# Performance work log

Measured on AMD Instinct MI355X. Metric: run time of the kernel, lower is better.

## Reference

```python
import jax, jax.numpy as jnp
import numpy as np

N_NODES = 100000
N_EDGES = 20000
N_PAIRS = 640000
IN_CH = 128
HEADS = 4
OUT_CH = 32


def setup_inputs() -> dict:
    key = jax.random.key(0)
    k1, k2, k3, k4, k5 = jax.random.split(key, 5)
    X = jax.random.normal(k1, (N_NODES, IN_CH), dtype=jnp.float32)
    # nn.Linear(in, H*C, bias=False); stored as [in, H*C] so X0 = X @ W
    W = jax.random.normal(k2, (IN_CH, HEADS * OUT_CH), dtype=jnp.float32) * (1.0 / np.sqrt(IN_CH))
    stdv = (6.0 / (HEADS + OUT_CH)) ** 0.5
    att_e = jax.random.uniform(k3, (1, HEADS, OUT_CH), dtype=jnp.float32, minval=-stdv, maxval=stdv)
    vertex = jax.random.randint(k4, (N_PAIRS,), 0, N_NODES, dtype=jnp.int64)
    edges = jax.random.randint(k5, (N_PAIRS,), 0, N_EDGES, dtype=jnp.int64)
    return {"X": X, "W": W, "att_e": att_e, "vertex": vertex, "edges": edges}


def reference(X, W, att_e, vertex, edges):
    N = X.shape[0]
    H, C = HEADS, OUT_CH
    X0 = X @ W                                  # [N, H*C]
    Xv_hc = X0.reshape(N, H, C)
    Xve = Xv_hc[vertex]                          # [M, H, C] gather
    # scatter-mean over hyperedges
    esum = jax.ops.segment_sum(Xve, edges, num_segments=N_EDGES)
    ecnt = jax.ops.segment_sum(jnp.ones((Xve.shape[0],), X.dtype), edges, num_segments=N_EDGES)
    Xe = esum / jnp.maximum(ecnt, 1.0)[:, None, None]   # [E, H, C]
    alpha_e = (Xe * att_e).sum(-1)               # [E, H]
    a_ev = alpha_e[edges]                        # [M, H]
    alpha = jax.nn.leaky_relu(a_ev, 0.01)
    # per-vertex softmax over incident hyperedges
    amax = jax.ops.segment_max(alpha, vertex, num_segments=N)
    alpha = jnp.exp(alpha - amax[vertex])
    asum = jax.ops.segment_sum(alpha, vertex, num_segments=N)
    alpha = alpha / (asum[vertex] + 1e-8)
    Xev = Xe[edges] * alpha[:, :, None]          # [M, H, C]
    Xv = jax.ops.segment_sum(Xev, vertex, num_segments=N)
    return Xv.reshape(N, H * C) + X0
```

## Files before the change

kernel.cpp:

```cpp
#include <hip/hip_runtime.h>
#include <hip/hip_bf16.h>

#define N_NODES 100000
#define N_EDGES 20000
#define N_PAIRS 640000
#define CH 128
#define HEADS 4
#define MAXDV 32

#define NG_GEMM 1563
#define NCHUNK 125
#define ECHUNK 5120
#define EW 5120
#define VWR 6250
#define NRANGE 4
#define VBIN_R 25000

#define OFF_X0H   0UL
#define OFF_XEH   25600000UL
#define OFF_LRE   30720000UL
#define OFF_LRV   31360000UL
#define OFF_BLKE  32000000UL
#define OFF_BLKV  34560000UL
#define OFF_GSE   47060000UL
#define OFF_GSV   47162400UL
#define OFF_WT    47662400UL
#define OFF_ALPHA 47695168UL
#define OFF_OFFE  48015168UL
#define OFF_ENDE  48097088UL
#define OFF_OFFV  48179008UL
#define OFF_ENDV  48579008UL
#define OFF_PIDXE 48979008UL
#define OFF_PIDXV 51539008UL
#define OFF_CNTE  54099008UL
#define OFF_CNTV  54180928UL
#define OFF_TOT   54580928UL
#define ZERO_BYTES 8UL

typedef __attribute__((ext_vector_type(8))) short bf16x8;
typedef __attribute__((ext_vector_type(4))) float f32x4;

__device__ inline short f2bf(float f) {
    __hip_bfloat16 h = __float2bfloat16(f);
    return reinterpret_cast<short&>(h);
}
__device__ inline float bf2f(short s) {
    unsigned int u = ((unsigned int)(unsigned short)s) << 16;
    union { unsigned int u; float f; } c; c.u = u;
    return c.f;
}

__global__ __launch_bounds__(256) void k_wprep(const float* __restrict__ W,
                                               short* __restrict__ Wt) {
    const int idx = blockIdx.x * 256 + threadIdx.x;
    const int n = idx >> 7, k = idx & 127;
    Wt[n * CH + k] = f2bf(W[k * CH + n]);
}

__device__ inline void gemm_body(int gb, const float* __restrict__ X,
                                 const short* __restrict__ Wt,
                                 short* __restrict__ X0h) {
    const int t = threadIdx.x;
    const int wave = t >> 6, lane = t & 63;
    const int r0 = gb * 64 + (wave >> 1) * 32;
    const int c0 = (wave & 1) * 64;
    const int lrow = lane & 15, lk8 = (lane >> 4) * 8;
    const int row0 = min(r0 + lrow, N_NODES - 1);
    const int row1 = min(r0 + 16 + lrow, N_NODES - 1);
    const float* px0 = &X[(size_t)row0 * CH + lk8];
    const float* px1 = &X[(size_t)row1 * CH + lk8];
    const short* pw0 = &Wt[(size_t)(c0 + lrow) * CH + lk8];

    f32x4 acc[2][4] = {};

    float4 xa[2][2]; bf16x8 bb[4];
    xa[0][0] = *(const float4*)(px0); xa[0][1] = *(const float4*)(px0 + 4);
    xa[1][0] = *(const float4*)(px1); xa[1][1] = *(const float4*)(px1 + 4);
#pragma unroll
    for (int n = 0; n < 4; ++n) bb[n] = *(const bf16x8*)(pw0 + n * 16 * CH);

#pragma unroll
    for (int kk = 0; kk < 4; ++kk) {
        float4 xn[2][2]; bf16x8 bn[4];
        if (kk < 3) {
            const int ks = (kk + 1) * 32;
            xn[0][0] = *(const float4*)(px0 + ks); xn[0][1] = *(const float4*)(px0 + ks + 4);
            xn[1][0] = *(const float4*)(px1 + ks); xn[1][1] = *(const float4*)(px1 + ks + 4);
#pragma unroll
            for (int n = 0; n < 4; ++n) bn[n] = *(const bf16x8*)(pw0 + n * 16 * CH + ks);
        }
        bf16x8 a[2];
#pragma unroll
        for (int m = 0; m < 2; ++m) {
            a[m][0] = f2bf(xa[m][0].x); a[m][1] = f2bf(xa[m][0].y);
            a[m][2] = f2bf(xa[m][0].z); a[m][3] = f2bf(xa[m][0].w);
            a[m][4] = f2bf(xa[m][1].x); a[m][5] = f2bf(xa[m][1].y);
            a[m][6] = f2bf(xa[m][1].z); a[m][7] = f2bf(xa[m][1].w);
        }
#pragma unroll
        for (int m = 0; m < 2; ++m)
#pragma unroll
            for (int n = 0; n < 4; ++n)
                acc[m][n] = __builtin_amdgcn_mfma_f32_16x16x32_bf16(a[m], bb[n], acc[m][n], 0, 0, 0);
        if (kk < 3) {
#pragma unroll
            for (int m = 0; m < 2; ++m) { xa[m][0] = xn[m][0]; xa[m][1] = xn[m][1]; }
#pragma unroll
            for (int n = 0; n < 4; ++n) bb[n] = bn[n];
        }
    }

#pragma unroll
    for (int m = 0; m < 2; ++m) {
#pragma unroll
        for (int reg = 0; reg < 4; ++reg) {
            const int row = r0 + m * 16 + (lane >> 4) * 4 + reg;
            if (row < N_NODES) {
#pragma unroll
                for (int n = 0; n < 4; ++n)
                    X0h[(size_t)row * CH + c0 + n * 16 + (lane & 15)] = f2bf(acc[m][n][reg]);
            }
        }
    }
}

__global__ __launch_bounds__(256) void k_phase1(const float* __restrict__ X,
                                                const short* __restrict__ Wt,
                                                short* __restrict__ X0h,
                                                const int* __restrict__ vertex,
                                                const int* __restrict__ edges,
                                                unsigned char* __restrict__ lrank_e,
                                                unsigned char* __restrict__ lrank_v,
                                                unsigned int* __restrict__ blkcnt_e,
                                                unsigned int* __restrict__ blkcnt_v) {
    __shared__ unsigned int hist[VWR];
    const int bid = blockIdx.x;
    const int t = threadIdx.x;

    if (bid < NRANGE * NCHUNK) {
        const int r = bid & 3, c = bid >> 2;
        for (int i = t; i < VWR; i += 256) hist[i] = 0;
        __syncthreads();
        const int base = c * ECHUNK;
        const int vmin = r * VBIN_R;
#pragma unroll
        for (int it = 0; it < 20; ++it) {
            const int m = base + it * 256 + t;
            const int loc = vertex[m] - vmin;
            if ((unsigned)loc < (unsigned)VBIN_R) {
                const unsigned sh = (unsigned)(loc & 3) * 8u;
                unsigned old = atomicAdd(&hist[loc >> 2], 1u << sh);
                lrank_v[m] = (unsigned char)((old >> sh) & 0xffu);
            }
        }
        __syncthreads();
        unsigned int* dst = &blkcnt_v[(size_t)(r * NCHUNK + c) * VWR];
        for (int w = t; w < VWR; w += 256) dst[w] = hist[w];
        return;
    }
    if (bid < NRANGE * NCHUNK + NCHUNK) {
        const int c = bid - NRANGE * NCHUNK;
        for (int i = t; i < EW; i += 256) hist[i] = 0;
        __syncthreads();
        const int base = c * ECHUNK;
#pragma unroll
        for (int it = 0; it < 20; ++it) {
            const int m = base + it * 256 + t;
            const int e = edges[m];
            const unsigned sh = (unsigned)(e & 3) * 8u;
            unsigned old = atomicAdd(&hist[e >> 2], 1u << sh);
            lrank_e[m] = (unsigned char)((old >> sh) & 0xffu);
        }
        __syncthreads();
        unsigned int* dst = &blkcnt_e[(size_t)c * EW];
        for (int w = t; w < EW; w += 256) dst[w] = hist[w];
        return;
    }
    gemm_body(bid - (NRANGE * NCHUNK + NCHUNK), X, Wt, X0h);
}

__global__ __launch_bounds__(256) void k_scan_p1(const unsigned int* __restrict__ blkcnt_e,
                                                 const unsigned int* __restrict__ blkcnt_v,
                                                 unsigned int* __restrict__ gse,
                                                 unsigned int* __restrict__ gsv) {
    const int bid = blockIdx.x;
    if (bid < 100) {
        const int gid = bid * 256 + threadIdx.x;
        const int g = gid / EW, w = gid % EW;
        unsigned s = 0;
#pragma unroll 5
        for (int i = 0; i < 25; ++i) s += blkcnt_e[(size_t)(g * 25 + i) * EW + w];
        gse[g * EW + w] = s;
        return;
    }
    const int vid = (bid - 100) * 256 + threadIdx.x;
    if (vid >= 20 * VWR) return;
    const int g = vid / VWR, w = vid % VWR;
    const int r = g / 5, cg = g % 5;
    unsigned s = 0;
#pragma unroll 5
    for (int i = 0; i < 25; ++i)
        s += blkcnt_v[(size_t)(r * NCHUNK + cg * 25 + i) * VWR + w];
    gsv[g * VWR + w] = s;
}

__global__ __launch_bounds__(256) void k_scan_p2(unsigned int* __restrict__ gse,
                                                 unsigned int* __restrict__ gsv,
                                                 int* __restrict__ cnt_e,
                                                 int* __restrict__ cnt_v) {
    const int bid = blockIdx.x;
    if (bid < 20) {
        const int w = bid * 256 + threadIdx.x;
        unsigned run = 0;
#pragma unroll
        for (int g = 0; g < 5; ++g) {
            unsigned c = gse[g * EW + w];
            gse[g * EW + w] = run;
            run += c;
        }
        int4 o = { (int)(run & 0xffu), (int)((run >> 8) & 0xffu),
                   (int)((run >> 16) & 0xffu), (int)(run >> 24) };
        *(int4*)&cnt_e[4 * w] = o;
        return;
    }
    const int id = (bid - 20) * 256 + threadIdx.x;
    if (id >= NRANGE * VWR) return;
    const int r = id / VWR, w = id % VWR;
    unsigned run = 0;
#pragma unroll
    for (int g = r * 5; g < r * 5 + 5; ++g) {
        unsigned c = gsv[g * VWR + w];
        gsv[g * VWR + w] = run;
        run += c;
    }
    int4 o = { (int)(run & 0xffu), (int)((run >> 8) & 0xffu),
               (int)((run >> 16) & 0xffu), (int)(run >> 24) };
    *(int4*)&cnt_v[r * VBIN_R + 4 * w] = o;
}

__global__ __launch_bounds__(256) void k_scan_p3(unsigned int* __restrict__ blkcnt_e,
                                                 unsigned int* __restrict__ blkcnt_v,
                                                 const unsigned int* __restrict__ gse,
                                                 const unsigned int* __restrict__ gsv) {
    const int bid = blockIdx.x;
    if (bid < 100) {
        const int gid = bid * 256 + threadIdx.x;
        const int g = gid / EW, w = gid % EW;
        unsigned run = gse[g * EW + w];
#pragma unroll 5
        for (int i = 0; i < 25; ++i) {
            const size_t idx = (size_t)(g * 25 + i) * EW + w;
            unsigned c = blkcnt_e[idx];
            blkcnt_e[idx] = run;
            run += c;
        }
        return;
    }
    const int vid = (bid - 100) * 256 + threadIdx.x;
    if (vid >= 20 * VWR) return;
    const int g = vid / VWR, w = vid % VWR;
    const int r = g / 5, cg = g % 5;
    unsigned run = gsv[g * VWR + w];
#pragma unroll 5
    for (int i = 0; i < 25; ++i) {
        const size_t idx = (size_t)(r * NCHUNK + cg * 25 + i) * VWR + w;
        unsigned c = blkcnt_v[idx];
        blkcnt_v[idx] = run;
        run += c;
    }
}

__global__ __launch_bounds__(256) void k_offsets2(const int* __restrict__ cnt_e,
                                                  int* __restrict__ off_e,
                                                  int* __restrict__ end_e,
                                                  const int* __restrict__ cnt_v,
                                                  int* __restrict__ off_v,
                                                  int* __restrict__ end_v,
                                                  int* __restrict__ totals) {
    __shared__ int s[256];
    __shared__ int base;
    const int bid = blockIdx.x, t = threadIdx.x;
    const int* cnt; int* off; int* end; int* total; int n, i;
    if (bid < 79) { cnt = cnt_e; off = off_e; end = end_e; total = &totals[0]; n = N_EDGES;  i = bid * 256 + t; }
    else          { cnt = cnt_v; off = off_v; end = end_v; total = &totals[1]; n = N_NODES; i = (bid - 79) * 256 + t; }
    const int c = (i < n) ? cnt[i] : 0;
    s[t] = c;
    __syncthreads();
    for (int d = 1; d < 256; d <<= 1) {
        int x = (t >= d) ? s[t - d] : 0;
        __syncthreads();
        s[t] += x;
        __syncthreads();
    }
    if (t == 0) base = atomicAdd(total, s[255]);
    __syncthreads();
    if (i < n) {
        int o = base + s[t] - c;
        off[i] = o;
        end[i] = o + c;
    }
}

__global__ __launch_bounds__(256) void k_scatter(const int* __restrict__ vertex,
                                                 const int* __restrict__ edges,
                                                 const unsigned char* __restrict__ lrank_e,
                                                 const unsigned char* __restrict__ lrank_v,
                                                 const unsigned int* __restrict__ blkcnt_e,
                                                 const unsigned int* __restrict__ blkcnt_v,
                                                 const int* __restrict__ off_e,
                                                 const int* __restrict__ off_v,
                                                 int* __restrict__ vlist_e,
                                                 int* __restrict__ elist_v) {
    const int m = blockIdx.x * 256 + threadIdx.x;
    const int e = edges[m];
    const int v = vertex[m];
    const int c = m / ECHUNK;
    const unsigned pe = blkcnt_e[(size_t)c * EW + (e >> 2)];
    const int er = (int)((pe >> ((unsigned)(e & 3) * 8u)) & 0xffu) + (int)lrank_e[m];
    const int r = v / VBIN_R, loc = v - r * VBIN_R;
    const unsigned pv = blkcnt_v[(size_t)(r * NCHUNK + c) * VWR + (loc >> 2)];
    const int vr = (int)((pv >> ((unsigned)(loc & 3) * 8u)) & 0xffu) + (int)lrank_v[m];
    vlist_e[off_e[e] + er] = v;
    elist_v[off_v[v] + vr] = e;
}

__global__ __launch_bounds__(256) void k_edge(const short* __restrict__ X0h,
                                              const int* __restrict__ off_e,
                                              const int* __restrict__ end_e,
                                              const int* __restrict__ vlist,
                                              const float* __restrict__ att,
                                              short* __restrict__ Xeh,
                                              float* __restrict__ alpha_le) {
    const int t = threadIdx.x;
    const int slot = t >> 5, lane = t & 31;
    const int half = lane >> 4, cl = lane & 15;
    const int e = blockIdx.x * 8 + slot;
    const int s = off_e[e], en = end_e[e];
    const int deg = en - s;

    float va[8] = {0.f, 0.f, 0.f, 0.f, 0.f, 0.f, 0.f, 0.f};
    for (int c0 = 0; c0 < deg; c0 += 32) {
        const int cn = min(32, deg - c0);
        int vl = (lane < cn) ? vlist[s + c0 + lane] : 0;
#pragma unroll 4
        for (int j = 0; j < cn; j += 2) {
            const int jj = j + half;
            const int vj = __shfl(vl, jj, 32);
            if (jj < cn) {
                bf16x8 x = *(const bf16x8*)&X0h[(size_t)vj * CH + cl * 8];
#pragma unroll
                for (int i = 0; i < 8; ++i) va[i] += bf2f(x[i]);
            }
        }
    }
#pragma unroll
    for (int i = 0; i < 8; ++i) va[i] += __shfl_xor(va[i], 16);

    const float invd = 1.0f / fmaxf((float)deg, 1.0f);
    bf16x8 xh;
    float xe[8];
#pragma unroll
    for (int i = 0; i < 8; ++i) { xe[i] = va[i] * invd; xh[i] = f2bf(xe[i]); }
    if (half == 0) *(bf16x8*)&Xeh[(size_t)e * CH + cl * 8] = xh;

    const float4 a0 = *(const float4*)&att[cl * 8];
    const float4 a1 = *(const float4*)&att[cl * 8 + 4];
    float p = xe[0] * a0.x + xe[1] * a0.y + xe[2] * a0.z + xe[3] * a0.w
            + xe[4] * a1.x + xe[5] * a1.y + xe[6] * a1.z + xe[7] * a1.w;
    p += __shfl_xor(p, 1);
    p += __shfl_xor(p, 2);
    if (half == 0 && (cl & 3) == 0) {
        alpha_le[e * HEADS + (cl >> 2)] = (p > 0.f) ? p : 0.01f * p;
    }
}

__global__ __launch_bounds__(256) void k_vertex(const short* __restrict__ X0h,
                                                const short* __restrict__ Xeh,
                                                const float* __restrict__ alpha_le,
                                                const int* __restrict__ off_v,
                                                const int* __restrict__ end_v,
                                                const int* __restrict__ elist,
                                                float* __restrict__ out) {
    const int t = threadIdx.x;
    const int slot = t >> 5, lane = t & 31;
    const int half = lane >> 4, cl = lane & 15, h = cl >> 2;
    const int v = blockIdx.x * 8 + slot;
    const int s = off_v[v], en = end_v[v];
    const int deg = en - s;

    __shared__ int   se[8][MAXDV];
    __shared__ float sa[8][MAXDV * HEADS];

    if (deg <= MAXDV && lane < deg) {
        int e = elist[s + lane];
        se[slot][lane] = e;
        *(float4*)&sa[slot][lane << 2] = *(const float4*)&alpha_le[e * HEADS];
    }
    const bf16x8 resh = *(const bf16x8*)&X0h[(size_t)v * CH + cl * 8];
    __syncthreads();

    float va[8] = {0.f, 0.f, 0.f, 0.f, 0.f, 0.f, 0.f, 0.f};
    if (deg <= MAXDV) {
        float mx = -INFINITY;
        for (int j = 0; j < deg; ++j) mx = fmaxf(mx, sa[slot][(j << 2) + h]);
        float ssum = 0.f;
        for (int j = 0; j < deg; ++j) ssum += __expf(sa[slot][(j << 2) + h] - mx);
        const float inv = 1.0f / (ssum + 1e-8f);
#pragma unroll 2
        for (int j = 0; j < deg; j += 2) {
            const int jj = j + half;
            if (jj < deg) {
                const float w = __expf(sa[slot][(jj << 2) + h] - mx) * inv;
                bf16x8 x = *(const bf16x8*)&Xeh[(size_t)se[slot][jj] * CH + cl * 8];
#pragma unroll
                for (int i = 0; i < 8; ++i) va[i] += w * bf2f(x[i]);
            }
        }
    } else {
        float mx = -INFINITY;
        for (int j = 0; j < deg; ++j) mx = fmaxf(mx, alpha_le[elist[s + j] * HEADS + h]);
        float ssum = 0.f;
        for (int j = 0; j < deg; ++j) ssum += __expf(alpha_le[elist[s + j] * HEADS + h] - mx);
        const float inv = 1.0f / (ssum + 1e-8f);
        for (int j = 0; j < deg; ++j) {
            if (half == 0) {
                const int e = elist[s + j];
                const float w = __expf(alpha_le[e * HEADS + h] - mx) * inv;
                bf16x8 x = *(const bf16x8*)&Xeh[(size_t)e * CH + cl * 8];
#pragma unroll
                for (int i = 0; i < 8; ++i) va[i] += w * bf2f(x[i]);
            }
        }
    }
#pragma unroll
    for (int i = 0; i < 8; ++i) va[i] += __shfl_xor(va[i], 16);

    if (half == 0) {
        float4 o0, o1;
        o0.x = va[0] + bf2f(resh[0]); o0.y = va[1] + bf2f(resh[1]);
        o0.z = va[2] + bf2f(resh[2]); o0.w = va[3] + bf2f(resh[3]);
        o1.x = va[4] + bf2f(resh[4]); o1.y = va[5] + bf2f(resh[5]);
        o1.z = va[6] + bf2f(resh[6]); o1.w = va[7] + bf2f(resh[7]);
        *(float4*)&out[(size_t)v * CH + cl * 8]     = o0;
        *(float4*)&out[(size_t)v * CH + cl * 8 + 4] = o1;
    }
}

extern "C" void kernel_launch(void* const* d_in, const int* in_sizes, int n_in,
                              void* d_out, int out_size, void* d_ws, size_t ws_size,
                              hipStream_t stream) {
    const float* X      = (const float*)d_in[0];
    const float* W      = (const float*)d_in[1];
    const float* att    = (const float*)d_in[2];
    const int*   vertex = (const int*)d_in[3];
    const int*   edges  = (const int*)d_in[4];
    float* out = (float*)d_out;

    char* ws = (char*)d_ws;
    short* X0h      = (short*)(ws + OFF_X0H);
    short* Xeh      = (short*)(ws + OFF_XEH);
    unsigned char* lrank_e = (unsigned char*)(ws + OFF_LRE);
    unsigned char* lrank_v = (unsigned char*)(ws + OFF_LRV);
    unsigned int*  blkcnt_e = (unsigned int*)(ws + OFF_BLKE);
    unsigned int*  blkcnt_v = (unsigned int*)(ws + OFF_BLKV);
    unsigned int*  gse      = (unsigned int*)(ws + OFF_GSE);
    unsigned int*  gsv      = (unsigned int*)(ws + OFF_GSV);
    short* Wt       = (short*)(ws + OFF_WT);
    float* alpha_le = (float*)(ws + OFF_ALPHA);
    int* off_e   = (int*)(ws + OFF_OFFE);
    int* end_e   = (int*)(ws + OFF_ENDE);
    int* off_v   = (int*)(ws + OFF_OFFV);
    int* end_v   = (int*)(ws + OFF_ENDV);
    int* vlist_e = (int*)(ws + OFF_PIDXE);
    int* elist_v = (int*)(ws + OFF_PIDXV);
    int* cnt_e   = (int*)(ws + OFF_CNTE);
    int* cnt_v   = (int*)(ws + OFF_CNTV);
    int* totals  = (int*)(ws + OFF_TOT);

    hipMemsetAsync(ws + OFF_TOT, 0, ZERO_BYTES, stream);

    k_wprep<<<64, 256, 0, stream>>>(W, Wt);
    k_phase1<<<NRANGE * NCHUNK + NCHUNK + NG_GEMM, 256, 0, stream>>>(
        X, Wt, X0h, vertex, edges, lrank_e, lrank_v, blkcnt_e, blkcnt_v);
    k_scan_p1<<<100 + 489, 256, 0, stream>>>(blkcnt_e, blkcnt_v, gse, gsv);
    k_scan_p2<<<20 + 98, 256, 0, stream>>>(gse, gsv, cnt_e, cnt_v);
    k_scan_p3<<<100 + 489, 256, 0, stream>>>(blkcnt_e, blkcnt_v, gse, gsv);
    k_offsets2<<<79 + 391, 256, 0, stream>>>(cnt_e, off_e, end_e, cnt_v, off_v, end_v, totals);
    k_scatter<<<N_PAIRS / 256, 256, 0, stream>>>(vertex, edges, lrank_e, lrank_v,
                                                 blkcnt_e, blkcnt_v, off_e, off_v,
                                                 vlist_e, elist_v);
    k_edge<<<N_EDGES / 8, 256, 0, stream>>>(X0h, off_e, end_e, vlist_e, att, Xeh, alpha_le);
    k_vertex<<<N_NODES / 8, 256, 0, stream>>>(X0h, Xeh, alpha_le, off_v, end_v, elist_v, out);
}
```

Before: 160.6 us.

## Split GEMM from counting kernel and compute vertex softmax with wave shuffles

```diff
diff --git a/kernel.cpp b/kernel.cpp
--- a/kernel.cpp
+++ b/kernel.cpp
@@ -44,10 +44,10 @@
     __hip_bfloat16 h = __float2bfloat16(f);
     return reinterpret_cast<short&>(h);
 }
+__device__ inline float bflo(unsigned w) { return __uint_as_float(w << 16); }
+__device__ inline float bfhi(unsigned w) { return __uint_as_float(w & 0xffff0000u); }
 __device__ inline float bf2f(short s) {
-    unsigned int u = ((unsigned int)(unsigned short)s) << 16;
-    union { unsigned int u; float f; } c; c.u = u;
-    return c.f;
+    return __uint_as_float(((unsigned)(unsigned short)s) << 16);
 }
 
 __global__ __launch_bounds__(256) void k_wprep(const float* __restrict__ W,
@@ -57,12 +57,12 @@
     Wt[n * CH + k] = f2bf(W[k * CH + n]);
 }
 
-__device__ inline void gemm_body(int gb, const float* __restrict__ X,
-                                 const short* __restrict__ Wt,
-                                 short* __restrict__ X0h) {
+__global__ __launch_bounds__(256) void k_gemm(const float* __restrict__ X,
+                                              const short* __restrict__ Wt,
+                                              short* __restrict__ X0h) {
     const int t = threadIdx.x;
     const int wave = t >> 6, lane = t & 63;
-    const int r0 = gb * 64 + (wave >> 1) * 32;
+    const int r0 = blockIdx.x * 64 + (wave >> 1) * 32;
     const int c0 = (wave & 1) * 64;
     const int lrow = lane & 15, lk8 = (lane >> 4) * 8;
     const int row0 = min(r0 + lrow, N_NODES - 1);
@@ -124,15 +124,12 @@
     }
 }
 
-__global__ __launch_bounds__(256) void k_phase1(const float* __restrict__ X,
-                                                const short* __restrict__ Wt,
-                                                short* __restrict__ X0h,
-                                                const int* __restrict__ vertex,
-                                                const int* __restrict__ edges,
-                                                unsigned char* __restrict__ lrank_e,
-                                                unsigned char* __restrict__ lrank_v,
-                                                unsigned int* __restrict__ blkcnt_e,
-                                                unsigned int* __restrict__ blkcnt_v) {
+__global__ __launch_bounds__(256) void k_count(const int* __restrict__ vertex,
+                                               const int* __restrict__ edges,
+                                               unsigned char* __restrict__ lrank_e,
+                                               unsigned char* __restrict__ lrank_v,
+                                               unsigned int* __restrict__ blkcnt_e,
+                                               unsigned int* __restrict__ blkcnt_v) {
     __shared__ unsigned int hist[VWR];
     const int bid = blockIdx.x;
     const int t = threadIdx.x;
@@ -158,25 +155,21 @@
         for (int w = t; w < VWR; w += 256) dst[w] = hist[w];
         return;
     }
-    if (bid < NRANGE * NCHUNK + NCHUNK) {
-        const int c = bid - NRANGE * NCHUNK;
-        for (int i = t; i < EW; i += 256) hist[i] = 0;
-        __syncthreads();
-        const int base = c * ECHUNK;
-#pragma unroll
-        for (int it = 0; it < 20; ++it) {
-            const int m = base + it * 256 + t;
-            const int e = edges[m];
-            const unsigned sh = (unsigned)(e & 3) * 8u;
-            unsigned old = atomicAdd(&hist[e >> 2], 1u << sh);
-            lrank_e[m] = (unsigned char)((old >> sh) & 0xffu);
-        }
-        __syncthreads();
-        unsigned int* dst = &blkcnt_e[(size_t)c * EW];
-        for (int w = t; w < EW; w += 256) dst[w] = hist[w];
-        return;
-    }
-    gemm_body(bid - (NRANGE * NCHUNK + NCHUNK), X, Wt, X0h);
+    const int c = bid - NRANGE * NCHUNK;
+    for (int i = t; i < EW; i += 256) hist[i] = 0;
+    __syncthreads();
+    const int base = c * ECHUNK;
+#pragma unroll
+    for (int it = 0; it < 20; ++it) {
+        const int m = base + it * 256 + t;
+        const int e = edges[m];
+        const unsigned sh = (unsigned)(e & 3) * 8u;
+        unsigned old = atomicAdd(&hist[e >> 2], 1u << sh);
+        lrank_e[m] = (unsigned char)((old >> sh) & 0xffu);
+    }
+    __syncthreads();
+    unsigned int* dst = &blkcnt_e[(size_t)c * EW];
+    for (int w = t; w < EW; w += 256) dst[w] = hist[w];
 }
 
 __global__ __launch_bounds__(256) void k_scan_p1(const unsigned int* __restrict__ blkcnt_e,
@@ -347,9 +340,11 @@
             const int jj = j + half;
             const int vj = __shfl(vl, jj, 32);
             if (jj < cn) {
-                bf16x8 x = *(const bf16x8*)&X0h[(size_t)vj * CH + cl * 8];
-#pragma unroll
-                for (int i = 0; i < 8; ++i) va[i] += bf2f(x[i]);
+                uint4 xq = *(const uint4*)&X0h[(size_t)vj * CH + cl * 8];
+                va[0] += bflo(xq.x); va[1] += bfhi(xq.x);
+                va[2] += bflo(xq.y); va[3] += bfhi(xq.y);
+                va[4] += bflo(xq.z); va[5] += bfhi(xq.z);
+                va[6] += bflo(xq.w); va[7] += bfhi(xq.w);
             }
         }
     }
@@ -391,29 +386,53 @@
     __shared__ int   se[8][MAXDV];
     __shared__ float sa[8][MAXDV * HEADS];
 
-    if (deg <= MAXDV && lane < deg) {
-        int e = elist[s + lane];
-        se[slot][lane] = e;
-        *(float4*)&sa[slot][lane << 2] = *(const float4*)&alpha_le[e * HEADS];
-    }
     const bf16x8 resh = *(const bf16x8*)&X0h[(size_t)v * CH + cl * 8];
-    __syncthreads();
 
     float va[8] = {0.f, 0.f, 0.f, 0.f, 0.f, 0.f, 0.f, 0.f};
     if (deg <= MAXDV) {
-        float mx = -INFINITY;
-        for (int j = 0; j < deg; ++j) mx = fmaxf(mx, sa[slot][(j << 2) + h]);
-        float ssum = 0.f;
-        for (int j = 0; j < deg; ++j) ssum += __expf(sa[slot][(j << 2) + h] - mx);
-        const float inv = 1.0f / (ssum + 1e-8f);
+        float4 al = make_float4(-INFINITY, -INFINITY, -INFINITY, -INFINITY);
+        if (lane < deg) {
+            const int e = elist[s + lane];
+            se[slot][lane] = e;
+            al = *(const float4*)&alpha_le[e * HEADS];
+        }
+        float4 mx = al;
+#pragma unroll
+        for (int msk = 1; msk < 32; msk <<= 1) {
+            mx.x = fmaxf(mx.x, __shfl_xor(mx.x, msk, 32));
+            mx.y = fmaxf(mx.y, __shfl_xor(mx.y, msk, 32));
+            mx.z = fmaxf(mx.z, __shfl_xor(mx.z, msk, 32));
+            mx.w = fmaxf(mx.w, __shfl_xor(mx.w, msk, 32));
+        }
+        float4 p = make_float4(0.f, 0.f, 0.f, 0.f);
+        if (lane < deg) {
+            p.x = __expf(al.x - mx.x); p.y = __expf(al.y - mx.y);
+            p.z = __expf(al.z - mx.z); p.w = __expf(al.w - mx.w);
+        }
+        float4 sm = p;
+#pragma unroll
+        for (int msk = 1; msk < 32; msk <<= 1) {
+            sm.x += __shfl_xor(sm.x, msk, 32);
+            sm.y += __shfl_xor(sm.y, msk, 32);
+            sm.z += __shfl_xor(sm.z, msk, 32);
+            sm.w += __shfl_xor(sm.w, msk, 32);
+        }
+        if (lane < deg) {
+            float4 w4;
+            w4.x = p.x / (sm.x + 1e-8f); w4.y = p.y / (sm.y + 1e-8f);
+            w4.z = p.z / (sm.z + 1e-8f); w4.w = p.w / (sm.w + 1e-8f);
+            *(float4*)&sa[slot][lane << 2] = w4;
+        }
 #pragma unroll 2
         for (int j = 0; j < deg; j += 2) {
             const int jj = j + half;
             if (jj < deg) {
-                const float w = __expf(sa[slot][(jj << 2) + h] - mx) * inv;
-                bf16x8 x = *(const bf16x8*)&Xeh[(size_t)se[slot][jj] * CH + cl * 8];
-#pragma unroll
-                for (int i = 0; i < 8; ++i) va[i] += w * bf2f(x[i]);
+                const float w = sa[slot][(jj << 2) + h];
+                uint4 xq = *(const uint4*)&Xeh[(size_t)se[slot][jj] * CH + cl * 8];
+                va[0] += w * bflo(xq.x); va[1] += w * bfhi(xq.x);
+                va[2] += w * bflo(xq.y); va[3] += w * bfhi(xq.y);
+                va[4] += w * bflo(xq.z); va[5] += w * bfhi(xq.z);
+                va[6] += w * bflo(xq.w); va[7] += w * bfhi(xq.w);
             }
         }
     } else {
@@ -426,9 +445,11 @@
             if (half == 0) {
                 const int e = elist[s + j];
                 const float w = __expf(alpha_le[e * HEADS + h] - mx) * inv;
-                bf16x8 x = *(const bf16x8*)&Xeh[(size_t)e * CH + cl * 8];
-#pragma unroll
-                for (int i = 0; i < 8; ++i) va[i] += w * bf2f(x[i]);
+                uint4 xq = *(const uint4*)&Xeh[(size_t)e * CH + cl * 8];
+                va[0] += w * bflo(xq.x); va[1] += w * bfhi(xq.x);
+                va[2] += w * bflo(xq.y); va[3] += w * bfhi(xq.y);
+                va[4] += w * bflo(xq.z); va[5] += w * bfhi(xq.z);
+                va[6] += w * bflo(xq.w); va[7] += w * bfhi(xq.w);
             }
         }
     }
@@ -480,8 +501,9 @@
     hipMemsetAsync(ws + OFF_TOT, 0, ZERO_BYTES, stream);
 
     k_wprep<<<64, 256, 0, stream>>>(W, Wt);
-    k_phase1<<<NRANGE * NCHUNK + NCHUNK + NG_GEMM, 256, 0, stream>>>(
-        X, Wt, X0h, vertex, edges, lrank_e, lrank_v, blkcnt_e, blkcnt_v);
+    k_count<<<NRANGE * NCHUNK + NCHUNK, 256, 0, stream>>>(
+        vertex, edges, lrank_e, lrank_v, blkcnt_e, blkcnt_v);
+    k_gemm<<<NG_GEMM, 256, 0, stream>>>(X, Wt, X0h);
     k_scan_p1<<<100 + 489, 256, 0, stream>>>(blkcnt_e, blkcnt_v, gse, gsv);
     k_scan_p2<<<20 + 98, 256, 0, stream>>>(gse, gsv, cnt_e, cnt_v);
     k_scan_p3<<<100 + 489, 256, 0, stream>>>(blkcnt_e, blkcnt_v, gse, gsv);
```

New measurement: 168.0 us. +4.7%, slower.

## Fuse offset scan into scan pass 2 and remap vertex kernel to half-warp per vertex

Applied to the files above, without the earlier changes.

```diff
diff --git a/kernel.cpp b/kernel.cpp
--- a/kernel.cpp
+++ b/kernel.cpp
@@ -32,8 +32,6 @@
 #define OFF_ENDV  48579008UL
 #define OFF_PIDXE 48979008UL
 #define OFF_PIDXV 51539008UL
-#define OFF_CNTE  54099008UL
-#define OFF_CNTV  54180928UL
 #define OFF_TOT   54580928UL
 #define ZERO_BYTES 8UL
 
@@ -44,10 +42,10 @@
     __hip_bfloat16 h = __float2bfloat16(f);
     return reinterpret_cast<short&>(h);
 }
+__device__ inline float bflo(unsigned w) { return __uint_as_float(w << 16); }
+__device__ inline float bfhi(unsigned w) { return __uint_as_float(w & 0xffff0000u); }
 __device__ inline float bf2f(short s) {
-    unsigned int u = ((unsigned int)(unsigned short)s) << 16;
-    union { unsigned int u; float f; } c; c.u = u;
-    return c.f;
+    return __uint_as_float(((unsigned)(unsigned short)s) << 16);
 }
 
 __global__ __launch_bounds__(256) void k_wprep(const float* __restrict__ W,
@@ -204,38 +202,67 @@
     gsv[g * VWR + w] = s;
 }
 
-__global__ __launch_bounds__(256) void k_scan_p2(unsigned int* __restrict__ gse,
-                                                 unsigned int* __restrict__ gsv,
-                                                 int* __restrict__ cnt_e,
-                                                 int* __restrict__ cnt_v) {
-    const int bid = blockIdx.x;
+__global__ __launch_bounds__(256) void k_p2o(unsigned int* __restrict__ gse,
+                                             unsigned int* __restrict__ gsv,
+                                             int* __restrict__ off_e,
+                                             int* __restrict__ end_e,
+                                             int* __restrict__ off_v,
+                                             int* __restrict__ end_v,
+                                             int* __restrict__ totals) {
+    __shared__ int s[256];
+    __shared__ int base;
+    const int bid = blockIdx.x, t = threadIdx.x;
+
+    unsigned run = 0;
+    int t0 = 0, t1 = 0, t2 = 0, t3 = 0;
+    int binbase = -1;
+    int* off; int* end; int* total;
+
     if (bid < 20) {
-        const int w = bid * 256 + threadIdx.x;
-        unsigned run = 0;
+        const int w = bid * 256 + t;
 #pragma unroll
         for (int g = 0; g < 5; ++g) {
             unsigned c = gse[g * EW + w];
             gse[g * EW + w] = run;
             run += c;
         }
-        int4 o = { (int)(run & 0xffu), (int)((run >> 8) & 0xffu),
-                   (int)((run >> 16) & 0xffu), (int)(run >> 24) };
-        *(int4*)&cnt_e[4 * w] = o;
-        return;
-    }
-    const int id = (bid - 20) * 256 + threadIdx.x;
-    if (id >= NRANGE * VWR) return;
-    const int r = id / VWR, w = id % VWR;
-    unsigned run = 0;
-#pragma unroll
-    for (int g = r * 5; g < r * 5 + 5; ++g) {
-        unsigned c = gsv[g * VWR + w];
-        gsv[g * VWR + w] = run;
-        run += c;
-    }
-    int4 o = { (int)(run & 0xffu), (int)((run >> 8) & 0xffu),
-               (int)((run >> 16) & 0xffu), (int)(run >> 24) };
-    *(int4*)&cnt_v[r * VBIN_R + 4 * w] = o;
+        t0 = run & 255; t1 = (run >> 8) & 255; t2 = (run >> 16) & 255; t3 = run >> 24;
+        binbase = 4 * w;
+        off = off_e; end = end_e; total = &totals[0];
+    } else {
+        const int id = (bid - 20) * 256 + t;
+        if (id < NRANGE * VWR) {
+            const int r = id / VWR, w = id % VWR;
+#pragma unroll
+            for (int g = r * 5; g < r * 5 + 5; ++g) {
+                unsigned c = gsv[g * VWR + w];
+                gsv[g * VWR + w] = run;
+                run += c;
+            }
+            t0 = run & 255; t1 = (run >> 8) & 255; t2 = (run >> 16) & 255; t3 = run >> 24;
+            binbase = r * VBIN_R + 4 * w;
+        }
+        off = off_v; end = end_v; total = &totals[1];
+    }
+
+    const int mysum = t0 + t1 + t2 + t3;
+    s[t] = mysum;
+    __syncthreads();
+    for (int d = 1; d < 256; d <<= 1) {
+        int x = (t >= d) ? s[t - d] : 0;
+        __syncthreads();
+        s[t] += x;
+        __syncthreads();
+    }
+    if (t == 0) base = atomicAdd(total, s[255]);
+    __syncthreads();
+    if (binbase >= 0) {
+        int b = base + s[t] - mysum;
+        off[binbase]     = b;           end[binbase]     = b + t0;  b += t0;
+        off[binbase + 1] = b;           end[binbase + 1] = b + t1;  b += t1;
+        off[binbase + 2] = b;           end[binbase + 2] = b + t2;  b += t2;
+        off[binbase + 3] = b;           end[binbase + 3] = b + t3;
+    }
 }
 
 __global__ __launch_bounds__(256) void k_scan_p3(unsigned int* __restrict__ blkcnt_e,
@@ -267,37 +294,6 @@
         unsigned c = blkcnt_v[idx];
         blkcnt_v[idx] = run;
         run += c;
-    }
-}
-
-__global__ __launch_bounds__(256) void k_offsets2(const int* __restrict__ cnt_e,
-                                                  int* __restrict__ off_e,
-                                                  int* __restrict__ end_e,
-                                                  const int* __restrict__ cnt_v,
-                                                  int* __restrict__ off_v,
-                                                  int* __restrict__ end_v,
-                                                  int* __restrict__ totals) {
-    __shared__ int s[256];
-    __shared__ int base;
-    const int bid = blockIdx.x, t = threadIdx.x;
-    const int* cnt; int* off; int* end; int* total; int n, i;
-    if (bid < 79) { cnt = cnt_e; off = off_e; end = end_e; total = &totals[0]; n = N_EDGES;  i = bid * 256 + t; }
-    else          { cnt = cnt_v; off = off_v; end = end_v; total = &totals[1]; n = N_NODES; i = (bid - 79) * 256 + t; }
-    const int c = (i < n) ? cnt[i] : 0;
-    s[t] = c;
-    __syncthreads();
-    for (int d = 1; d < 256; d <<= 1) {
-        int x = (t >= d) ? s[t - d] : 0;
-        __syncthreads();
-        s[t] += x;
-        __syncthreads();
-    }
-    if (t == 0) base = atomicAdd(total, s[255]);
-    __syncthreads();
-    if (i < n) {
-        int o = base + s[t] - c;
-        off[i] = o;
-        end[i] = o + c;
     }
 }
 
@@ -337,19 +333,22 @@
     const int e = blockIdx.x * 8 + slot;
     const int s = off_e[e], en = end_e[e];
     const int deg = en - s;
+    const short* __restrict__ xb = X0h + cl * 8;
 
     float va[8] = {0.f, 0.f, 0.f, 0.f, 0.f, 0.f, 0.f, 0.f};
     for (int c0 = 0; c0 < deg; c0 += 32) {
         const int cn = min(32, deg - c0);
-        int vl = (lane < cn) ? vlist[s + c0 + lane] : 0;
+        int vl = (lane < cn) ? (vlist[s + c0 + lane] << 7) : 0;
 #pragma unroll 4
         for (int j = 0; j < cn; j += 2) {
             const int jj = j + half;
-            const int vj = __shfl(vl, jj, 32);
+            const int vo = __shfl(vl, jj, 32);
             if (jj < cn) {
-                bf16x8 x = *(const bf16x8*)&X0h[(size_t)vj * CH + cl * 8];
-#pragma unroll
-                for (int i = 0; i < 8; ++i) va[i] += bf2f(x[i]);
+                uint4 xq = *(const uint4*)(xb + vo);
+                va[0] += bflo(xq.x); va[1] += bfhi(xq.x);
+                va[2] += bflo(xq.y); va[3] += bfhi(xq.y);
+                va[4] += bflo(xq.z); va[5] += bfhi(xq.z);
+                va[6] += bflo(xq.w); va[7] += bfhi(xq.w);
             }
         }
     }
@@ -383,38 +382,35 @@
                                                 float* __restrict__ out) {
     const int t = threadIdx.x;
     const int slot = t >> 5, lane = t & 31;
-    const int half = lane >> 4, cl = lane & 15, h = cl >> 2;
-    const int v = blockIdx.x * 8 + slot;
+    const int grp = lane >> 4, cl = lane & 15, h = cl >> 2;
+    const int v = blockIdx.x * 16 + slot * 2 + grp;
     const int s = off_v[v], en = end_v[v];
     const int deg = en - s;
 
-    __shared__ int   se[8][MAXDV];
-    __shared__ float sa[8][MAXDV * HEADS];
-
-    if (deg <= MAXDV && lane < deg) {
-        int e = elist[s + lane];
-        se[slot][lane] = e;
-        *(float4*)&sa[slot][lane << 2] = *(const float4*)&alpha_le[e * HEADS];
-    }
-    const bf16x8 resh = *(const bf16x8*)&X0h[(size_t)v * CH + cl * 8];
-    __syncthreads();
+    __shared__ int   se[8][2][MAXDV];
+    __shared__ float sa[8][2][MAXDV * HEADS];
+
+    const short* __restrict__ xb = Xeh + cl * 8;
 
     float va[8] = {0.f, 0.f, 0.f, 0.f, 0.f, 0.f, 0.f, 0.f};
     if (deg <= MAXDV) {
+        for (int j = cl; j < deg; j += 16) {
+            const int e = elist[s + j];
+            se[slot][grp][j] = e << 7;
+            *(float4*)&sa[slot][grp][j << 2] = *(const float4*)&alpha_le[e * HEADS];
+        }
         float mx = -INFINITY;
-        for (int j = 0; j < deg; ++j) mx = fmaxf(mx, sa[slot][(j << 2) + h]);
+        for (int j = 0; j < deg; ++j) mx = fmaxf(mx, sa[slot][grp][(j << 2) + h]);
         float ssum = 0.f;
-        for (int j = 0; j < deg; ++j) ssum += __expf(sa[slot][(j << 2) + h] - mx);
+        for (int j = 0; j < deg; ++j) ssum += __expf(sa[slot][grp][(j << 2) + h] - mx);
         const float inv = 1.0f / (ssum + 1e-8f);
-#pragma unroll 2
-        for (int j = 0; j < deg; j += 2) {
-            const int jj = j + half;
-            if (jj < deg) {
-                const float w = __expf(sa[slot][(jj << 2) + h] - mx) * inv;
-                bf16x8 x = *(const bf16x8*)&Xeh[(size_t)se[slot][jj] * CH + cl * 8];
-#pragma unroll
-                for (int i = 0; i < 8; ++i) va[i] += w * bf2f(x[i]);
-            }
+        for (int j = 0; j < deg; ++j) {
+            const float w = __expf(sa[slot][grp][(j << 2) + h] - mx) * inv;
+            uint4 xq = *(const uint4*)(xb + se[slot][grp][j]);
+            va[0] += w * bflo(xq.x); va[1] += w * bfhi(xq.x);
+            va[2] += w * bflo(xq.y); va[3] += w * bfhi(xq.y);
+            va[4] += w * bflo(xq.z); va[5] += w * bfhi(xq.z);
+            va[6] += w * bflo(xq.w); va[7] += w * bfhi(xq.w);
         }
     } else {
         float mx = -INFINITY;
@@ -423,27 +419,24 @@
         for (int j = 0; j < deg; ++j) ssum += __expf(alpha_le[elist[s + j] * HEADS + h] - mx);
         const float inv = 1.0f / (ssum + 1e-8f);
         for (int j = 0; j < deg; ++j) {
-            if (half == 0) {
-                const int e = elist[s + j];
-                const float w = __expf(alpha_le[e * HEADS + h] - mx) * inv;
-                bf16x8 x = *(const bf16x8*)&Xeh[(size_t)e * CH + cl * 8];
-#pragma unroll
-                for (int i = 0; i < 8; ++i) va[i] += w * bf2f(x[i]);
-            }
-        }
-    }
-#pragma unroll
-    for (int i = 0; i < 8; ++i) va[i] += __shfl_xor(va[i], 16);
-
-    if (half == 0) {
-        float4 o0, o1;
-        o0.x = va[0] + bf2f(resh[0]); o0.y = va[1] + bf2f(resh[1]);
-        o0.z = va[2] + bf2f(resh[2]); o0.w = va[3] + bf2f(resh[3]);
-        o1.x = va[4] + bf2f(resh[4]); o1.y = va[5] + bf2f(resh[5]);
-        o1.z = va[6] + bf2f(resh[6]); o1.w = va[7] + bf2f(resh[7]);
-        *(float4*)&out[(size_t)v * CH + cl * 8]     = o0;
-        *(float4*)&out[(size_t)v * CH + cl * 8 + 4] = o1;
-    }
+            const int e = elist[s + j];
+            const float w = __expf(alpha_le[e * HEADS + h] - mx) * inv;
+            uint4 xq = *(const uint4*)(xb + (e << 7));
+            va[0] += w * bflo(xq.x); va[1] += w * bfhi(xq.x);
+            va[2] += w * bflo(xq.y); va[3] += w * bfhi(xq.y);
+            va[4] += w * bflo(xq.z); va[5] += w * bfhi(xq.z);
+            va[6] += w * bflo(xq.w); va[7] += w * bfhi(xq.w);
+        }
+    }
+
+    const uint4 rq = *(const uint4*)&X0h[(size_t)v * CH + cl * 8];
+    float4 o0, o1;
+    o0.x = va[0] + bflo(rq.x); o0.y = va[1] + bfhi(rq.x);
+    o0.z = va[2] + bflo(rq.y); o0.w = va[3] + bfhi(rq.y);
+    o1.x = va[4] + bflo(rq.z); o1.y = va[5] + bfhi(rq.z);
+    o1.z = va[6] + bflo(rq.w); o1.w = va[7] + bfhi(rq.w);
+    *(float4*)&out[(size_t)v * CH + cl * 8]     = o0;
+    *(float4*)&out[(size_t)v * CH + cl * 8 + 4] = o1;
 }
 
 extern "C" void kernel_launch(void* const* d_in, const int* in_sizes, int n_in,
@@ -473,8 +466,6 @@
     int* end_v   = (int*)(ws + OFF_ENDV);
     int* vlist_e = (int*)(ws + OFF_PIDXE);
     int* elist_v = (int*)(ws + OFF_PIDXV);
-    int* cnt_e   = (int*)(ws + OFF_CNTE);
-    int* cnt_v   = (int*)(ws + OFF_CNTV);
     int* totals  = (int*)(ws + OFF_TOT);
 
     hipMemsetAsync(ws + OFF_TOT, 0, ZERO_BYTES, stream);
@@ -483,12 +474,11 @@
     k_phase1<<<NRANGE * NCHUNK + NCHUNK + NG_GEMM, 256, 0, stream>>>(
         X, Wt, X0h, vertex, edges, lrank_e, lrank_v, blkcnt_e, blkcnt_v);
     k_scan_p1<<<100 + 489, 256, 0, stream>>>(blkcnt_e, blkcnt_v, gse, gsv);
-    k_scan_p2<<<20 + 98, 256, 0, stream>>>(gse, gsv, cnt_e, cnt_v);
+    k_p2o<<<20 + 98, 256, 0, stream>>>(gse, gsv, off_e, end_e, off_v, end_v, totals);
     k_scan_p3<<<100 + 489, 256, 0, stream>>>(blkcnt_e, blkcnt_v, gse, gsv);
-    k_offsets2<<<79 + 391, 256, 0, stream>>>(cnt_e, off_e, end_e, cnt_v, off_v, end_v, totals);
     k_scatter<<<N_PAIRS / 256, 256, 0, stream>>>(vertex, edges, lrank_e, lrank_v,
                                                  blkcnt_e, blkcnt_v, off_e, off_v,
                                                  vlist_e, elist_v);
     k_edge<<<N_EDGES / 8, 256, 0, stream>>>(X0h, off_e, end_e, vlist_e, att, Xeh, alpha_le);
-    k_vertex<<<N_NODES / 8, 256, 0, stream>>>(X0h, Xeh, alpha_le, off_v, end_v, elist_v, out);
-}
+    k_vertex<<<N_NODES / 16, 256, 0, stream>>>(X0h, Xeh, alpha_le, off_v, end_v, elist_v, out);
+}
```

After: 146.4 us. 1.1x faster.
